# Kernel optimization log

Measured on AMD Instinct MI355X. Metric: run time of the kernel, lower is better.

Reference implementation:

```python
import jax, jax.numpy as jnp
import numpy as np

N, K, NC, D = 32768, 4096, 4, 256


def setup_inputs() -> dict:
    key = jax.random.key(0)
    k1, k2, k3 = jax.random.split(key, 3)
    x = jax.random.normal(k1, (N, D), dtype=jnp.float32)
    mu = jax.random.normal(k2, (K, NC, D), dtype=jnp.float32)
    # std must be positive (it is inverted); uniform in [0.5, 1.5)
    std = jax.random.uniform(k3, (D,), dtype=jnp.float32) + 0.5
    return {"x": x, "mu": mu, "std": std}


def reference(x, mu, std):
    # Gaussian density eval: exp(-0.5 * sum_d (x_nd - mu_k0d)^2 / std_d)
    # Expanded algebraically to avoid the (N, K, D) intermediate:
    #   ||x - mu||^2_w = x^2 . w + mu^2 . w - 2 * x . (mu * w),  w = 1/std
    inv_std = 1.0 / std                       # (D,)
    mu0 = mu[:, 0, :]                          # (K, D) -- only component 0 is used
    x_sq = jnp.einsum("nd,d->n", x * x, inv_std)          # (N,)
    mu_sq = jnp.einsum("kd,d->k", mu0 * mu0, inv_std)     # (K,)
    cross = jnp.einsum("nd,kd->nk", x, mu0 * inv_std)     # (N, K) GEMM
    logits = -0.5 * (x_sq[:, None] + mu_sq[None, :] - 2.0 * cross)
    return jnp.exp(logits)                                 # (N, K)
```

## Files before the change

kernel.cpp:

```cpp
#include <hip/hip_runtime.h>

#define N_ 32768
#define K_ 4096
#define NC_ 4
#define D_ 256

using floatx4 = __attribute__((ext_vector_type(4))) float;
using bf16x8  = __attribute__((ext_vector_type(8))) short;

__device__ __forceinline__ unsigned short f2bf(float f) {
  union { float f; unsigned u; } a;
  a.f = f;
  unsigned u = a.u;
  u += 0x7fffu + ((u >> 16) & 1u);
  return (unsigned short)(u >> 16);
}

__device__ __forceinline__ void async_copy16(void* lds, const void* g) {
  __builtin_amdgcn_global_load_lds(
      (__attribute__((address_space(1))) void*)(g),
      (__attribute__((address_space(3))) void*)(lds),
      16, 0, 0);
}

template <bool WRITE_BF>
__global__ void prep_x_kern(const float* __restrict__ x, const float* __restrict__ sd,
                            unsigned short* __restrict__ xb, float* __restrict__ xsq) {
  const int lane = threadIdx.x & 63;
  const int row  = blockIdx.x * 4 + (threadIdx.x >> 6);
  const float4 xv = reinterpret_cast<const float4*>(x + (size_t)row * D_)[lane];
  const float4 sv = reinterpret_cast<const float4*>(sd)[lane];
  const float i0 = 1.0f / sv.x, i1 = 1.0f / sv.y, i2 = 1.0f / sv.z, i3 = 1.0f / sv.w;
  float s = xv.x * xv.x * i0 + xv.y * xv.y * i1 + xv.z * xv.z * i2 + xv.w * xv.w * i3;
  if (WRITE_BF) {
    union { unsigned short u[4]; uint2 v; } p;
    p.u[0] = f2bf(xv.x); p.u[1] = f2bf(xv.y); p.u[2] = f2bf(xv.z); p.u[3] = f2bf(xv.w);
    reinterpret_cast<uint2*>(xb)[(size_t)row * 64 + lane] = p.v;
  }
#pragma unroll
  for (int off = 32; off > 0; off >>= 1) s += __shfl_down(s, off, 64);
  if (lane == 0) xsq[row] = s;
}

template <bool WRITE_BF>
__global__ void prep_mu_kern(const float* __restrict__ mu, const float* __restrict__ sd,
                             unsigned short* __restrict__ bb, float* __restrict__ musq) {
  const int lane = threadIdx.x & 63;
  const int row  = blockIdx.x * 4 + (threadIdx.x >> 6);
  const float4 mv = reinterpret_cast<const float4*>(mu + (size_t)row * (NC_ * D_))[lane];
  const float4 sv = reinterpret_cast<const float4*>(sd)[lane];
  const float i0 = 1.0f / sv.x, i1 = 1.0f / sv.y, i2 = 1.0f / sv.z, i3 = 1.0f / sv.w;
  float s = mv.x * mv.x * i0 + mv.y * mv.y * i1 + mv.z * mv.z * i2 + mv.w * mv.w * i3;
  if (WRITE_BF) {
    union { unsigned short u[4]; uint2 v; } p;
    p.u[0] = f2bf(mv.x * i0); p.u[1] = f2bf(mv.y * i1);
    p.u[2] = f2bf(mv.z * i2); p.u[3] = f2bf(mv.w * i3);
    reinterpret_cast<uint2*>(bb)[(size_t)row * 64 + lane] = p.v;
  }
#pragma unroll
  for (int off = 32; off > 0; off >>= 1) s += __shfl_down(s, off, 64);
  if (lane == 0) musq[row] = s;
}

__global__ __launch_bounds__(256, 3) void gauss_mfma(
    const unsigned short* __restrict__ xb, const unsigned short* __restrict__ bb,
    const float* __restrict__ xsq, const float* __restrict__ musq,
    float* __restrict__ out) {
  constexpr int BM = 128, BN = 128, BK = 32;
  __shared__ __align__(16) unsigned short As[BM * BK];
  __shared__ __align__(16) unsigned short Bs[BN * BK];
  const int tid  = threadIdx.x;
  const int wave = tid >> 6, lane = tid & 63;
  const int wm = wave >> 1, wn = wave & 1;

  const int b   = blockIdx.x;
  const int xcd = b & 7;
  const int g   = b >> 3;
  const int rowT = (xcd << 5) | (g & 31);
  const int colT = g >> 5;
  const int rowBase = rowT * BM;
  const int colBase = colT * BN;

  const int srow = lane >> 2;
  const int scol = (lane & 3) * 8;
  const unsigned short* gA0 = xb + (size_t)(rowBase + wave * 16 + srow) * D_ + scol;
  const unsigned short* gA1 = gA0 + (size_t)64 * D_;
  const unsigned short* gB0 = bb + (size_t)(colBase + wave * 16 + srow) * D_ + scol;
  const unsigned short* gB1 = gB0 + (size_t)64 * D_;
  unsigned short* lA0 = &As[(wave * 16) * BK];
  unsigned short* lA1 = &As[(wave * 16 + 64) * BK];
  unsigned short* lB0 = &Bs[(wave * 16) * BK];
  unsigned short* lB1 = &Bs[(wave * 16 + 64) * BK];

  floatx4 acc[4][4] = {};
  const int fr = lane & 15;
  const int fk = (lane >> 4) * 8;

#pragma unroll
  for (int kt = 0; kt < D_ / BK; ++kt) {
    __syncthreads();
    async_copy16(lA0, gA0 + kt * BK);
    async_copy16(lA1, gA1 + kt * BK);
    async_copy16(lB0, gB0 + kt * BK);
    async_copy16(lB1, gB1 + kt * BK);
    __syncthreads();
    bf16x8 af[4], bfv[4];
#pragma unroll
    for (int i = 0; i < 4; ++i)
      af[i] = *reinterpret_cast<const bf16x8*>(&As[(wm * 64 + i * 16 + fr) * BK + fk]);
#pragma unroll
    for (int j = 0; j < 4; ++j)
      bfv[j] = *reinterpret_cast<const bf16x8*>(&Bs[(wn * 64 + j * 16 + fr) * BK + fk]);
#pragma unroll
    for (int i = 0; i < 4; ++i)
#pragma unroll
      for (int j = 0; j < 4; ++j)
        acc[i][j] = __builtin_amdgcn_mfma_f32_16x16x32_bf16(af[i], bfv[j], acc[i][j], 0, 0, 0);
  }

  const int q = lane >> 4, c = lane & 15;
  float ms[4];
#pragma unroll
  for (int j = 0; j < 4; ++j) ms[j] = musq[colBase + wn * 64 + j * 16 + c];
#pragma unroll
  for (int i = 0; i < 4; ++i) {
#pragma unroll
    for (int r = 0; r < 4; ++r) {
      const int row = rowBase + wm * 64 + i * 16 + q * 4 + r;
      const float xs = xsq[row];
      float* orow = out + (size_t)row * K_ + colBase + wn * 64 + c;
#pragma unroll
      for (int j = 0; j < 4; ++j)
        __builtin_nontemporal_store(__expf(acc[i][j][r] - 0.5f * (xs + ms[j])),
                                    orow + j * 16);
    }
  }
}

__global__ void gauss_mfma_fused(const float* __restrict__ x, const float* __restrict__ mu,
                                 const float* __restrict__ sd,
                                 const float* __restrict__ xsq, const float* __restrict__ musq,
                                 float* __restrict__ out) {
  constexpr int BM = 128, BN = 128, BK = 32;
  __shared__ __align__(16) unsigned short As[BM * BK];
  __shared__ __align__(16) unsigned short Bs[BN * BK];
  __shared__ float invs[D_];
  const int tid = threadIdx.x;
  invs[tid] = 1.0f / sd[tid];
  const int wave = tid >> 6, lane = tid & 63;
  const int wm = wave >> 1, wn = wave & 1;
  const int rowBase = blockIdx.y * BM;
  const int colBase = blockIdx.x * BN;
  const int srow = tid >> 1;
  const int scol = (tid & 1) * 16;
  const float* gA = x + (size_t)(rowBase + srow) * D_ + scol;
  const float* gB = mu + (size_t)(colBase + srow) * (NC_ * D_) + scol;
  __syncthreads();

  floatx4 acc[4][4] = {};
  const int fr = lane & 15;
  const int fk = (lane >> 4) * 8;

  for (int kt = 0; kt < D_ / BK; ++kt) {
    const int k0 = kt * BK;
    float4 a0 = *(const float4*)(gA + k0);
    float4 a1 = *(const float4*)(gA + k0 + 4);
    float4 a2 = *(const float4*)(gA + k0 + 8);
    float4 a3 = *(const float4*)(gA + k0 + 12);
    float4 b0 = *(const float4*)(gB + k0);
    float4 b1 = *(const float4*)(gB + k0 + 4);
    float4 b2 = *(const float4*)(gB + k0 + 8);
    float4 b3 = *(const float4*)(gB + k0 + 12);
    float fa[16] = {a0.x, a0.y, a0.z, a0.w, a1.x, a1.y, a1.z, a1.w,
                    a2.x, a2.y, a2.z, a2.w, a3.x, a3.y, a3.z, a3.w};
    float fb[16] = {b0.x, b0.y, b0.z, b0.w, b1.x, b1.y, b1.z, b1.w,
                    b2.x, b2.y, b2.z, b2.w, b3.x, b3.y, b3.z, b3.w};
    union { unsigned short u[8]; uint4 v; } pa0, pa1, pb0, pb1;
#pragma unroll
    for (int t = 0; t < 8; ++t) {
      pa0.u[t] = f2bf(fa[t]);
      pa1.u[t] = f2bf(fa[t + 8]);
      pb0.u[t] = f2bf(fb[t] * invs[k0 + scol + t]);
      pb1.u[t] = f2bf(fb[t + 8] * invs[k0 + scol + t + 8]);
    }
    __syncthreads();
    *(uint4*)&As[srow * BK + scol]     = pa0.v;
    *(uint4*)&As[srow * BK + scol + 8] = pa1.v;
    *(uint4*)&Bs[srow * BK + scol]     = pb0.v;
    *(uint4*)&Bs[srow * BK + scol + 8] = pb1.v;
    __syncthreads();
    bf16x8 af[4], bfv[4];
#pragma unroll
    for (int i = 0; i < 4; ++i)
      af[i] = *reinterpret_cast<const bf16x8*>(&As[(wm * 64 + i * 16 + fr) * BK + fk]);
#pragma unroll
    for (int j = 0; j < 4; ++j)
      bfv[j] = *reinterpret_cast<const bf16x8*>(&Bs[(wn * 64 + j * 16 + fr) * BK + fk]);
#pragma unroll
    for (int i = 0; i < 4; ++i)
#pragma unroll
      for (int j = 0; j < 4; ++j)
        acc[i][j] = __builtin_amdgcn_mfma_f32_16x16x32_bf16(af[i], bfv[j], acc[i][j], 0, 0, 0);
  }

  const int q = lane >> 4, c = lane & 15;
  float ms[4];
#pragma unroll
  for (int j = 0; j < 4; ++j) ms[j] = musq[colBase + wn * 64 + j * 16 + c];
#pragma unroll
  for (int i = 0; i < 4; ++i) {
#pragma unroll
    for (int r = 0; r < 4; ++r) {
      const int row = rowBase + wm * 64 + i * 16 + q * 4 + r;
      const float xs = xsq[row];
      float* orow = out + (size_t)row * K_ + colBase + wn * 64 + c;
#pragma unroll
      for (int j = 0; j < 4; ++j)
        orow[j * 16] = __expf(acc[i][j][r] - 0.5f * (xs + ms[j]));
    }
  }
}

__global__ void gauss_naive(const float* __restrict__ x, const float* __restrict__ mu,
                            const float* __restrict__ sd, float* __restrict__ out) {
  const int k = blockIdx.x * 256 + threadIdx.x;
  const int n = blockIdx.y;
  const float* xr = x + (size_t)n * D_;
  const float* mr = mu + (size_t)k * (NC_ * D_);
  float s = 0.0f;
  for (int d = 0; d < D_; ++d) {
    const float diff = xr[d] - mr[d];
    s += diff * diff / sd[d];
  }
  out[(size_t)n * K_ + k] = __expf(-0.5f * s);
}

extern "C" void kernel_launch(void* const* d_in, const int* in_sizes, int n_in,
                              void* d_out, int out_size, void* d_ws, size_t ws_size,
                              hipStream_t stream) {
  const float* x  = (const float*)d_in[0];
  const float* mu = (const float*)d_in[1];
  const float* sd = (const float*)d_in[2];
  float* out = (float*)d_out;

  const size_t xb_bytes   = (size_t)N_ * D_ * 2;
  const size_t bb_bytes   = (size_t)K_ * D_ * 2;
  const size_t xsq_bytes  = (size_t)N_ * 4;
  const size_t musq_bytes = (size_t)K_ * 4;

  if (ws_size >= xb_bytes + bb_bytes + xsq_bytes + musq_bytes) {
    unsigned short* xb = (unsigned short*)d_ws;
    unsigned short* bb = (unsigned short*)((char*)d_ws + xb_bytes);
    float* xsq  = (float*)((char*)d_ws + xb_bytes + bb_bytes);
    float* musq = (float*)((char*)d_ws + xb_bytes + bb_bytes + xsq_bytes);
    prep_x_kern<true><<<N_ / 4, 256, 0, stream>>>(x, sd, xb, xsq);
    prep_mu_kern<true><<<K_ / 4, 256, 0, stream>>>(mu, sd, bb, musq);
    gauss_mfma<<<(N_ / 128) * (K_ / 128), 256, 0, stream>>>(xb, bb, xsq, musq, out);
  } else if (ws_size >= xsq_bytes + musq_bytes) {
    float* xsq  = (float*)d_ws;
    float* musq = (float*)((char*)d_ws + xsq_bytes);
    prep_x_kern<false><<<N_ / 4, 256, 0, stream>>>(x, sd, nullptr, xsq);
    prep_mu_kern<false><<<K_ / 4, 256, 0, stream>>>(mu, sd, nullptr, musq);
    gauss_mfma_fused<<<dim3(K_ / 128, N_ / 128), 256, 0, stream>>>(x, mu, sd, xsq, musq, out);
  } else {
    gauss_naive<<<dim3(K_ / 256, N_), 256, 0, stream>>>(x, mu, sd, out);
  }
}
```

Before: 591.9 us.

## Keep a 128-row A band resident in LDS and loop over column tiles

```diff
diff --git a/kernel.cpp b/kernel.cpp
--- a/kernel.cpp
+++ b/kernel.cpp
@@ -62,77 +62,84 @@
   if (lane == 0) musq[row] = s;
 }
 
-__global__ __launch_bounds__(256, 3) void gauss_mfma(
+__global__ __launch_bounds__(256, 2) void gauss_chain(
     const unsigned short* __restrict__ xb, const unsigned short* __restrict__ bb,
     const float* __restrict__ xsq, const float* __restrict__ musq,
     float* __restrict__ out) {
-  constexpr int BM = 128, BN = 128, BK = 32;
-  __shared__ __align__(16) unsigned short As[BM * BK];
-  __shared__ __align__(16) unsigned short Bs[BN * BK];
+  constexpr int BK = 32;
+  constexpr int CHUNK = 128 * BK;
+  __shared__ __align__(16) unsigned short As[8 * CHUNK];
   const int tid  = threadIdx.x;
   const int wave = tid >> 6, lane = tid & 63;
   const int wm = wave >> 1, wn = wave & 1;
 
-  const int b   = blockIdx.x;
-  const int xcd = b & 7;
-  const int g   = b >> 3;
-  const int rowT = (xcd << 5) | (g & 31);
-  const int colT = g >> 5;
-  const int rowBase = rowT * BM;
-  const int colBase = colT * BN;
+  const int b    = blockIdx.x;
+  const int xcd  = b & 7;
+  const int g    = b >> 3;
+  const int band = (xcd << 5) | (g & 31);
+  const int half = g >> 5;
+  const int rowBase  = band * 128;
+  const int colBase0 = half * 2048;
 
   const int srow = lane >> 2;
   const int scol = (lane & 3) * 8;
   const unsigned short* gA0 = xb + (size_t)(rowBase + wave * 16 + srow) * D_ + scol;
   const unsigned short* gA1 = gA0 + (size_t)64 * D_;
-  const unsigned short* gB0 = bb + (size_t)(colBase + wave * 16 + srow) * D_ + scol;
-  const unsigned short* gB1 = gB0 + (size_t)64 * D_;
   unsigned short* lA0 = &As[(wave * 16) * BK];
   unsigned short* lA1 = &As[(wave * 16 + 64) * BK];
-  unsigned short* lB0 = &Bs[(wave * 16) * BK];
-  unsigned short* lB1 = &Bs[(wave * 16 + 64) * BK];
-
-  floatx4 acc[4][4] = {};
+#pragma unroll
+  for (int kt = 0; kt < 8; ++kt) {
+    async_copy16(lA0 + kt * CHUNK, gA0 + kt * BK);
+    async_copy16(lA1 + kt * CHUNK, gA1 + kt * BK);
+  }
+  __syncthreads();
+
   const int fr = lane & 15;
   const int fk = (lane >> 4) * 8;
-
-#pragma unroll
-  for (int kt = 0; kt < D_ / BK; ++kt) {
-    __syncthreads();
-    async_copy16(lA0, gA0 + kt * BK);
-    async_copy16(lA1, gA1 + kt * BK);
-    async_copy16(lB0, gB0 + kt * BK);
-    async_copy16(lB1, gB1 + kt * BK);
-    __syncthreads();
-    bf16x8 af[4], bfv[4];
-#pragma unroll
-    for (int i = 0; i < 4; ++i)
-      af[i] = *reinterpret_cast<const bf16x8*>(&As[(wm * 64 + i * 16 + fr) * BK + fk]);
-#pragma unroll
-    for (int j = 0; j < 4; ++j)
-      bfv[j] = *reinterpret_cast<const bf16x8*>(&Bs[(wn * 64 + j * 16 + fr) * BK + fk]);
-#pragma unroll
-    for (int i = 0; i < 4; ++i)
+  const int q  = lane >> 4, c = lane & 15;
+
+  float xs[4][4];
+#pragma unroll
+  for (int i = 0; i < 4; ++i)
+#pragma unroll
+    for (int r = 0; r < 4; ++r)
+      xs[i][r] = xsq[rowBase + wm * 64 + i * 16 + q * 4 + r];
+
+  for (int ct = 0; ct < 16; ++ct) {
+    const int colBase = colBase0 + ct * 128;
+    const unsigned short* Bbase = bb + (size_t)(colBase + wn * 64 + fr) * D_ + fk;
+    floatx4 acc[4][4] = {};
+#pragma unroll
+    for (int kt = 0; kt < 8; ++kt) {
+      bf16x8 bfv[4];
 #pragma unroll
       for (int j = 0; j < 4; ++j)
-        acc[i][j] = __builtin_amdgcn_mfma_f32_16x16x32_bf16(af[i], bfv[j], acc[i][j], 0, 0, 0);
-  }
-
-  const int q = lane >> 4, c = lane & 15;
-  float ms[4];
-#pragma unroll
-  for (int j = 0; j < 4; ++j) ms[j] = musq[colBase + wn * 64 + j * 16 + c];
-#pragma unroll
-  for (int i = 0; i < 4; ++i) {
-#pragma unroll
-    for (int r = 0; r < 4; ++r) {
-      const int row = rowBase + wm * 64 + i * 16 + q * 4 + r;
-      const float xs = xsq[row];
-      float* orow = out + (size_t)row * K_ + colBase + wn * 64 + c;
-#pragma unroll
-      for (int j = 0; j < 4; ++j)
-        __builtin_nontemporal_store(__expf(acc[i][j][r] - 0.5f * (xs + ms[j])),
-                                    orow + j * 16);
+        bfv[j] = *reinterpret_cast<const bf16x8*>(Bbase + (size_t)(j * 16) * D_ + kt * BK);
+      bf16x8 af[4];
+#pragma unroll
+      for (int i = 0; i < 4; ++i)
+        af[i] = *reinterpret_cast<const bf16x8*>(
+            &As[kt * CHUNK + (wm * 64 + i * 16 + fr) * BK + fk]);
+#pragma unroll
+      for (int i = 0; i < 4; ++i)
+#pragma unroll
+        for (int j = 0; j < 4; ++j)
+          acc[i][j] = __builtin_amdgcn_mfma_f32_16x16x32_bf16(af[i], bfv[j], acc[i][j], 0, 0, 0);
+    }
+    float ms[4];
+#pragma unroll
+    for (int j = 0; j < 4; ++j) ms[j] = musq[colBase + wn * 64 + j * 16 + c];
+#pragma unroll
+    for (int i = 0; i < 4; ++i) {
+#pragma unroll
+      for (int r = 0; r < 4; ++r) {
+        const int row = rowBase + wm * 64 + i * 16 + q * 4 + r;
+        float* orow = out + (size_t)row * K_ + colBase + wn * 64 + c;
+#pragma unroll
+        for (int j = 0; j < 4; ++j)
+          __builtin_nontemporal_store(__expf(acc[i][j][r] - 0.5f * (xs[i][r] + ms[j])),
+                                      orow + j * 16);
+      }
     }
   }
 }
@@ -255,7 +262,7 @@
     float* musq = (float*)((char*)d_ws + xb_bytes + bb_bytes + xsq_bytes);
     prep_x_kern<true><<<N_ / 4, 256, 0, stream>>>(x, sd, xb, xsq);
     prep_mu_kern<true><<<K_ / 4, 256, 0, stream>>>(mu, sd, bb, musq);
-    gauss_mfma<<<(N_ / 128) * (K_ / 128), 256, 0, stream>>>(xb, bb, xsq, musq, out);
+    gauss_chain<<<512, 256, 0, stream>>>(xb, bb, xsq, musq, out);
   } else if (ws_size >= xsq_bytes + musq_bytes) {
     float* xsq  = (float*)d_ws;
     float* musq = (float*)((char*)d_ws + xsq_bytes);
```

After: 650.2 us. 9.9% more time.
